# Kernel tuning notes

Hardware: AMD Instinct MI355X
Metric: run time of the kernel (lower is better)

Reference implementation:

```python
import jax, jax.numpy as jnp
import numpy as np

N, D, F = 20000, 16, 3  # nodes, receptive-field size (degree), feature dim


def setup_inputs() -> dict:
    key = jax.random.key(0)
    k1, k2 = jax.random.split(key)
    # per-node feature tensors: first CCN layer, parts[i]={i}, so tensors[i] is [1,1,F] -> squeezed to [F]
    tensors = jax.random.normal(k1, (N, F), dtype=jnp.float32)
    # padded receptive fields: neigh[i] = child node indices with adjM[i, j] == 1
    neigh = jnp.sort(jax.random.randint(k2, (N, D), 0, N), axis=1)
    return {"tensors": tensors, "neigh": neigh}


def reference(tensors, neigh):
    # new_parts[i] = ordered union of children's (singleton) parts = sorted neighbor ids
    new_parts = jnp.sort(neigh, axis=1)  # [N, D]
    # chi[i, c, a] = 1 iff new_parts[i][a] == parts[neigh[i,c]][0] == neigh[i,c]
    # (the alternativePermutationMatrix_AToB in1d test, for singleton child parts)
    chi = (new_parts[:, None, :] == neigh[:, :, None]).astype(tensors.dtype)  # [N, D(child c), D(slot a)]
    # gather each child's feature tensor T[j,k,s] with j=k=1 -> [N, D, F]
    feat = tensors[neigh]
    # promotion einsum 'aj,bk,jks->abs' with |j|=|k|=1, batched over node i and child c
    promotions = jnp.einsum('nca,ncb,ncs->ncabs', chi, chi, feat)  # [N, D, D, D, F]
    return promotions, new_parts
```

## Files before the change

### kernel.cpp

```cpp
#include <hip/hip_runtime.h>


constexpr int NN = 20000;
constexpr int DD = 16;
constexpr int FF = 3;
constexpr int PROMO_PER_NODE = DD * DD * DD * FF;
constexpr long long PROMO_TOTAL = (long long)NN * PROMO_PER_NODE;

__global__ __launch_bounds__(192) void ccn_promote_kernel(
    const float* __restrict__ tensors,
    const int* __restrict__ neigh,
    float* __restrict__ out)
{
    const int n = blockIdx.x;
    const int t = threadIdx.x;

    const int* nrow = neigh + (size_t)n * DD;

    if (t < DD) {
        out[(size_t)PROMO_TOTAL + (size_t)n * DD + t] = (float)nrow[t];
    }

    const int a  = t / 12;
    const int k  = t - a * 12;
    const int e0 = 4 * k;
    const int b0 = (e0 + 0) / 3, s0 = (e0 + 0) % 3;
    const int b1 = (e0 + 1) / 3, s1 = (e0 + 1) % 3;
    const int b2 = (e0 + 2) / 3, s2 = (e0 + 2) % 3;
    const int b3 = (e0 + 3) / 3, s3 = (e0 + 3) % 3;

    const int nva  = nrow[a];
    const int nvb0 = nrow[b0];
    const int nvb1 = nrow[b1];
    const int nvb2 = nrow[b2];
    const int nvb3 = nrow[b3];

    const bool x0 = (s0 == 0), x1 = (s0 == 1);
    const bool y0 = (s1 == 0), y1 = (s1 == 1);
    const bool z0 = (s2 == 0), z1 = (s2 == 1);
    const bool w0 = (s3 == 0), w1 = (s3 == 1);

    int   mc[DD];
    float g0[DD], g1[DD], g2[DD];
#pragma unroll
    for (int c = 0; c < DD; ++c) {
        mc[c] = __builtin_amdgcn_readfirstlane(nrow[c]);
    }
#pragma unroll
    for (int c = 0; c < DD; ++c) {
        const float* src = tensors + (size_t)mc[c] * FF;
        g0[c] = src[0];
        g1[c] = src[1];
        g2[c] = src[2];
    }

    float4* outv = reinterpret_cast<float4*>(out + (size_t)n * PROMO_PER_NODE) + t;

#pragma unroll
    for (int c = 0; c < DD; ++c) {
        const int m = mc[c];
        const float fx = x0 ? g0[c] : (x1 ? g1[c] : g2[c]);
        const float fy = y0 ? g0[c] : (y1 ? g1[c] : g2[c]);
        const float fz = z0 ? g0[c] : (z1 ? g1[c] : g2[c]);
        const float fw = w0 ? g0[c] : (w1 ? g1[c] : g2[c]);
        const bool ca = (nva == m);
        float4 v;
        v.x = (ca && (nvb0 == m)) ? fx : 0.0f;
        v.y = (ca && (nvb1 == m)) ? fy : 0.0f;
        v.z = (ca && (nvb2 == m)) ? fz : 0.0f;
        v.w = (ca && (nvb3 == m)) ? fw : 0.0f;
        outv[c * 192] = v;
    }
}

extern "C" void kernel_launch(void* const* d_in, const int* in_sizes, int n_in,
                              void* d_out, int out_size, void* d_ws, size_t ws_size,
                              hipStream_t stream) {
    const float* tensors = (const float*)d_in[0];
    const int*   neigh   = (const int*)d_in[1];
    float*       out     = (float*)d_out;

    ccn_promote_kernel<<<NN, 192, 0, stream>>>(tensors, neigh, out);
}
```

Measured before the change: 972.1 us.

## Assign four nodes per wavefront with persistent-style loop and vectorized neighbor loads

Restructures the work split so each 64-lane wavefront processes four whole nodes sequentially, each lane handling three float4 column groups, instead of one 192-thread block per node. Neighbor rows are loaded as int4 vectors and broadcast with readfirstlane, and the per-lane index math is hoisted out of the node loop. This cuts the block count and per-block setup overhead for a store-bound kernel, but it gives less parallelism per node and a longer serial chain per wave.

```diff
diff --git a/kernel.cpp b/kernel.cpp
--- a/kernel.cpp
+++ b/kernel.cpp
@@ -7,69 +7,85 @@
 constexpr int PROMO_PER_NODE = DD * DD * DD * FF;
 constexpr long long PROMO_TOTAL = (long long)NN * PROMO_PER_NODE;
 
-__global__ __launch_bounds__(192) void ccn_promote_kernel(
+constexpr int TPB    = 128;
+constexpr int BLOCKS = 2500;
+constexpr int NPW    = 4;
+
+#define RFL(x) __builtin_amdgcn_readfirstlane(x)
+
+__global__ __launch_bounds__(TPB) void ccn_promote_kernel(
     const float* __restrict__ tensors,
-    const int* __restrict__ neigh,
-    float* __restrict__ out)
+    const int*   __restrict__ neigh,
+    float*       __restrict__ out)
 {
-    const int n = blockIdx.x;
-    const int t = threadIdx.x;
+    const int lane = threadIdx.x & 63;
+    const int wv   = RFL(blockIdx.x * (TPB / 64) + (threadIdx.x >> 6));
 
-    const int* nrow = neigh + (size_t)n * DD;
-
-    if (t < DD) {
-        out[(size_t)PROMO_TOTAL + (size_t)n * DD + t] = (float)nrow[t];
+    int aa[3], b0[3], b1[3], b2[3], b3[3], s0[3], s1[3], s2[3], s3[3];
+#pragma unroll
+    for (int j = 0; j < 3; ++j) {
+        const int t  = j * 64 + lane;
+        const int a  = t / 12;
+        const int k  = t - a * 12;
+        const int e0 = 4 * k;
+        aa[j] = a;
+        b0[j] = (e0 + 0) / 3; s0[j] = (e0 + 0) % 3;
+        b1[j] = (e0 + 1) / 3; s1[j] = (e0 + 1) % 3;
+        b2[j] = (e0 + 2) / 3; s2[j] = (e0 + 2) % 3;
+        b3[j] = (e0 + 3) / 3; s3[j] = (e0 + 3) % 3;
     }
 
-    const int a  = t / 12;
-    const int k  = t - a * 12;
-    const int e0 = 4 * k;
-    const int b0 = (e0 + 0) / 3, s0 = (e0 + 0) % 3;
-    const int b1 = (e0 + 1) / 3, s1 = (e0 + 1) % 3;
-    const int b2 = (e0 + 2) / 3, s2 = (e0 + 2) % 3;
-    const int b3 = (e0 + 3) / 3, s3 = (e0 + 3) % 3;
+#pragma unroll 1
+    for (int i = 0; i < NPW; ++i) {
+        const int n = wv * NPW + i;
+        const int* nrow = neigh + (size_t)n * DD;
 
-    const int nva  = nrow[a];
-    const int nvb0 = nrow[b0];
-    const int nvb1 = nrow[b1];
-    const int nvb2 = nrow[b2];
-    const int nvb3 = nrow[b3];
+        const int4 r0 = ((const int4*)nrow)[0];
+        const int4 r1 = ((const int4*)nrow)[1];
+        const int4 r2 = ((const int4*)nrow)[2];
+        const int4 r3 = ((const int4*)nrow)[3];
+        int mc[DD];
+        mc[ 0]=RFL(r0.x); mc[ 1]=RFL(r0.y); mc[ 2]=RFL(r0.z); mc[ 3]=RFL(r0.w);
+        mc[ 4]=RFL(r1.x); mc[ 5]=RFL(r1.y); mc[ 6]=RFL(r1.z); mc[ 7]=RFL(r1.w);
+        mc[ 8]=RFL(r2.x); mc[ 9]=RFL(r2.y); mc[10]=RFL(r2.z); mc[11]=RFL(r2.w);
+        mc[12]=RFL(r3.x); mc[13]=RFL(r3.y); mc[14]=RFL(r3.z); mc[15]=RFL(r3.w);
 
-    const bool x0 = (s0 == 0), x1 = (s0 == 1);
-    const bool y0 = (s1 == 0), y1 = (s1 == 1);
-    const bool z0 = (s2 == 0), z1 = (s2 == 1);
-    const bool w0 = (s3 == 0), w1 = (s3 == 1);
+        if (lane < DD)
+            out[PROMO_TOTAL + (size_t)n * DD + lane] = (float)nrow[lane];
 
-    int   mc[DD];
-    float g0[DD], g1[DD], g2[DD];
+        int va[3], vb0[3], vb1[3], vb2[3], vb3[3];
 #pragma unroll
-    for (int c = 0; c < DD; ++c) {
-        mc[c] = __builtin_amdgcn_readfirstlane(nrow[c]);
-    }
+        for (int j = 0; j < 3; ++j) {
+            va [j] = nrow[aa[j]];
+            vb0[j] = nrow[b0[j]];
+            vb1[j] = nrow[b1[j]];
+            vb2[j] = nrow[b2[j]];
+            vb3[j] = nrow[b3[j]];
+        }
+
+        float f0[DD], f1[DD], f2[DD];
 #pragma unroll
-    for (int c = 0; c < DD; ++c) {
-        const float* src = tensors + (size_t)mc[c] * FF;
-        g0[c] = src[0];
-        g1[c] = src[1];
-        g2[c] = src[2];
-    }
+        for (int c = 0; c < DD; ++c) {
+            const float* src = tensors + (size_t)mc[c] * FF;
+            f0[c] = src[0]; f1[c] = src[1]; f2[c] = src[2];
+        }
 
-    float4* outv = reinterpret_cast<float4*>(out + (size_t)n * PROMO_PER_NODE) + t;
-
+        float4* outv = reinterpret_cast<float4*>(out + (size_t)n * PROMO_PER_NODE);
 #pragma unroll
-    for (int c = 0; c < DD; ++c) {
-        const int m = mc[c];
-        const float fx = x0 ? g0[c] : (x1 ? g1[c] : g2[c]);
-        const float fy = y0 ? g0[c] : (y1 ? g1[c] : g2[c]);
-        const float fz = z0 ? g0[c] : (z1 ? g1[c] : g2[c]);
-        const float fw = w0 ? g0[c] : (w1 ? g1[c] : g2[c]);
-        const bool ca = (nva == m);
-        float4 v;
-        v.x = (ca && (nvb0 == m)) ? fx : 0.0f;
-        v.y = (ca && (nvb1 == m)) ? fy : 0.0f;
-        v.z = (ca && (nvb2 == m)) ? fz : 0.0f;
-        v.w = (ca && (nvb3 == m)) ? fw : 0.0f;
-        outv[c * 192] = v;
+        for (int c = 0; c < DD; ++c) {
+            const int   m  = mc[c];
+            const float g0 = f0[c], g1 = f1[c], g2 = f2[c];
+#pragma unroll
+            for (int j = 0; j < 3; ++j) {
+                const bool ca = (va[j] == m);
+                float4 v;
+                v.x = (ca && (vb0[j] == m)) ? (s0[j]==0 ? g0 : (s0[j]==1 ? g1 : g2)) : 0.0f;
+                v.y = (ca && (vb1[j] == m)) ? (s1[j]==0 ? g0 : (s1[j]==1 ? g1 : g2)) : 0.0f;
+                v.z = (ca && (vb2[j] == m)) ? (s2[j]==0 ? g0 : (s2[j]==1 ? g1 : g2)) : 0.0f;
+                v.w = (ca && (vb3[j] == m)) ? (s3[j]==0 ? g0 : (s3[j]==1 ? g1 : g2)) : 0.0f;
+                outv[c * 192 + j * 64 + lane] = v;
+            }
+        }
     }
 }
 
@@ -80,5 +96,5 @@
     const int*   neigh   = (const int*)d_in[1];
     float*       out     = (float*)d_out;
 
-    ccn_promote_kernel<<<NN, 192, 0, stream>>>(tensors, neigh, out);
+    ccn_promote_kernel<<<BLOCKS, TPB, 0, stream>>>(tensors, neigh, out);
 }
```

New measurement: 974.1 us. No clear change (+0.2%).
